# Optimization experiments

Measured on AMD Instinct MI355X. Metric: run time of the kernel, lower is better.

## Reference

```python
import jax, jax.numpy as jnp
import numpy as np
import math

D_MODEL = 256
N_HEAD = 1
C_IN = 32
B, L = 8, 2048
FACTOR = 5


def _pos_encoding(L, D):
    pos = jnp.arange(L, dtype=jnp.float32)[:, None]
    div = jnp.exp(jnp.arange(0, D, 2, dtype=jnp.float32) * (-math.log(10000.0) / D))
    pe = jnp.zeros((L, D), dtype=jnp.float32)
    pe = pe.at[:, 0::2].set(jnp.sin(pos * div))
    pe = pe.at[:, 1::2].set(jnp.cos(pos * div))
    return pe


def _layer_norm(x, g, b, eps=1e-5):
    mu = x.mean(-1, keepdims=True)
    var = ((x - mu) ** 2).mean(-1, keepdims=True)
    return (x - mu) / jnp.sqrt(var + eps) * g + b


def setup_inputs():
    key = jax.random.key(0)
    ks = jax.random.split(key, 16)
    D = D_MODEL
    s = 0.02
    p = {}
    p["x"] = jax.random.normal(ks[0], (B, L, C_IN), jnp.float32)
    sample_k = min(FACTOR * math.ceil(math.log(L)), L)  # = 40 for L=2048
    p["sample_idx"] = jax.random.randint(ks[1], (L, sample_k), 0, L)
    p["emb_w"] = jax.random.normal(ks[2], (C_IN, N_HEAD * D)) * s
    p["emb_b"] = jnp.zeros((N_HEAD * D,))
    for i, n in enumerate(["wq", "wk", "wv", "wo"]):
        p[n] = jax.random.normal(ks[3 + i], (D, D)) * s
        p["b" + n[1]] = jnp.zeros((D,))
    p["conv1_w"] = jax.random.normal(ks[7], (D, D)) * s  # Conv1d kernel=1 == linear, d_ff = d_model
    p["conv1_b"] = jnp.zeros((D,))
    p["conv2_w"] = jax.random.normal(ks[8], (D, D)) * s
    p["conv2_b"] = jnp.zeros((D,))
    for n in ["ln1", "ln2", "lnf"]:
        p[n + "_g"] = jnp.ones((D,))
        p[n + "_b"] = jnp.zeros((D,))
    p["gru_wih"] = jax.random.normal(ks[9], (3 * D, D)) * s
    p["gru_whh"] = jax.random.normal(ks[10], (3 * D, D)) * s
    p["gru_bih"] = jnp.zeros((3 * D,))
    p["gru_bhh"] = jnp.zeros((3 * D,))
    p["fc_w"] = jax.random.normal(ks[11], (D, 1)) * s
    p["fc_b"] = jnp.zeros((1,))
    return p


def _forward(x, sample_idx, emb_w, emb_b, wq, bq, wk, bk, wv, bv, wo, bo,
             conv1_w, conv1_b, conv2_w, conv2_b, ln1_g, ln1_b, ln2_g, ln2_b,
             lnf_g, lnf_b, gru_wih, gru_whh, gru_bih, gru_bhh, fc_w, fc_b):
    Bx, Lx, _ = x.shape
    H = N_HEAD
    src = x @ emb_w + emb_b + _pos_encoding(Lx, emb_w.shape[1])  # [B,L,D]
    D = src.shape[-1]
    dk = D // H

    def heads(t, w, b):
        return (t @ w + b).reshape(Bx, Lx, H, dk).transpose(0, 2, 1, 3)  # [B,H,L,dk]

    Q = heads(src, wq, bq)
    K = heads(src, wk, bk)
    V = heads(src, wv, bv)

    # ---- ProbSparse attention (Informer, non-masked) ----
    u = sample_idx.shape[1]                                  # n_top == sample_k here
    K_sample = K[:, :, sample_idx, :]                        # [B,H,L,s,dk]
    QK_s = jnp.einsum("bhld,bhlsd->bhls", Q, K_sample)
    M = QK_s.max(-1) - QK_s.sum(-1) / Lx                     # sparsity measure per query
    _, top = jax.lax.top_k(M, u)                             # [B,H,u]
    Q_red = jnp.take_along_axis(Q, top[..., None], axis=2)   # [B,H,u,dk]
    scores = jnp.einsum("bhud,bhkd->bhuk", Q_red, K) / jnp.sqrt(jnp.float32(dk))
    attn = jax.nn.softmax(scores, axis=-1)
    upd = jnp.einsum("bhuk,bhkd->bhud", attn, V)             # [B,H,u,dk]
    ctx = jnp.broadcast_to(V.mean(axis=2, keepdims=True), Q.shape)  # initial context = mean(V)
    bi = jnp.arange(Bx)[:, None, None]
    hi = jnp.arange(H)[None, :, None]
    ctx = ctx.at[bi, hi, top].set(upd)
    out = ctx.transpose(0, 2, 1, 3).reshape(Bx, Lx, D) @ wo + bo

    # ---- EncoderLayer FFN (Conv1d k=1 -> gelu -> Conv1d k=1), residuals, norms ----
    x1 = _layer_norm(src + out, ln1_g, ln1_b)
    y = jax.nn.gelu(x1 @ conv1_w + conv1_b, approximate=False)
    y = y @ conv2_w + conv2_b
    enc = _layer_norm(_layer_norm(x1 + y, ln2_g, ln2_b), lnf_g, lnf_b)

    # ---- GRU: faithful to source bug: seq-major nn.GRU fed [B,L,D] -> scans over batch dim ----
    def step(h, xt):
        gi = xt @ gru_wih.T + gru_bih
        gh = h @ gru_whh.T + gru_bhh
        ir, iz, inn = jnp.split(gi, 3, axis=-1)
        hr, hz, hn = jnp.split(gh, 3, axis=-1)
        r = jax.nn.sigmoid(ir + hr)
        z = jax.nn.sigmoid(iz + hz)
        n = jnp.tanh(inn + r * hn)
        h = (1.0 - z) * n + z * h
        return h, h

    h0 = jnp.zeros((Lx, enc.shape[-1]), enc.dtype)
    _, gru_out = jax.lax.scan(step, h0, enc)  # [B,L,D]
    return gru_out[:, -1, :] @ fc_w + fc_b    # [B,1]


def reference(x, sample_idx, emb_w, emb_b, wq, bq, wk, bk, wv, bv, wo, bo,
              conv1_w, conv1_b, conv2_w, conv2_b, ln1_g, ln1_b, ln2_g, ln2_b,
              lnf_g, lnf_b, gru_wih, gru_whh, gru_bih, gru_bhh, fc_w, fc_b):
    return _forward(x, sample_idx, emb_w, emb_b, wq, bq, wk, bk, wv, bv, wo, bo,
                    conv1_w, conv1_b, conv2_w, conv2_b, ln1_g, ln1_b, ln2_g, ln2_b,
                    lnf_g, lnf_b, gru_wih, gru_whh, gru_bih, gru_bhh, fc_w, fc_b)
```

## Files before the change

kernel.cpp:

```cpp
#include <hip/hip_runtime.h>
#include <hip/hip_bf16.h>
#include <math.h>

#define BB 8
#define LL 2048
#define CIN 32
#define DD 256
#define UU 40
#define NROW (BB*LL)
#define NSL  (NROW*DD)
#define GB 8

typedef unsigned short u16;
typedef __attribute__((ext_vector_type(8))) short short8;
typedef __attribute__((ext_vector_type(4))) float f32x4;

__device__ __forceinline__ u16 f2bf(float v) {
    unsigned u = __float_as_uint(v);
    unsigned r = (u + 0x7FFF + ((u >> 16) & 1)) >> 16;
    return (u16)r;
}
__device__ __forceinline__ float bf2f(u16 h) {
    return __uint_as_float(((unsigned)h) << 16);
}

template<int CTRL>
__device__ __forceinline__ float dpp_add(float v) {
    int s = __builtin_amdgcn_update_dpp(0, __float_as_int(v), CTRL, 0xf, 0xf, true);
    return v + __int_as_float(s);
}
__device__ __forceinline__ float row16_sum(float v) {
    v = dpp_add<0x118>(v);
    v = dpp_add<0x114>(v);
    v = dpp_add<0x112>(v);
    v = dpp_add<0x111>(v);
    return v;
}
__device__ __forceinline__ float dot4(float4 a, float4 b) {
    return a.x * b.x + a.y * b.y + a.z * b.z + a.w * b.w;
}

__global__ __launch_bounds__(256) void src_kernel(
    const float* __restrict__ x, const float* __restrict__ emb_w,
    const float* __restrict__ emb_b,
    u16* __restrict__ srch, u16* __restrict__ srcl, float* __restrict__ srcrow)
{
    __shared__ float xs[CIN];
    const int orig = blockIdx.x;
    const int b = orig & 7;
    const int l = orig >> 3;
    const int r = (b << 11) | l;
    const int d = threadIdx.x;
    if (d < CIN) xs[d] = x[(size_t)r * CIN + d];
    __syncthreads();
    float acc = emb_b[d];
#pragma unroll 8
    for (int c = 0; c < CIN; ++c) acc += xs[c] * emb_w[c * DD + d];
    const int i = d >> 1;
    const float ang = (float)l * expf((float)(2 * i) * (-9.210340371976184f / 256.0f));
    const float pe = (d & 1) ? cosf(ang) : sinf(ang);
    const float v = acc + pe;
    const u16 h = f2bf(v);
    srch[(size_t)r * DD + d] = h;
    srcl[(size_t)r * DD + d] = f2bf(v - bf2f(h));
    if (l == LL - 1) srcrow[b * DD + d] = v;
}

__global__ __launch_bounds__(256) void splitw_kernel(
    const float* __restrict__ wq, const float* __restrict__ wk,
    const float* __restrict__ wv, u16* __restrict__ whT, u16* __restrict__ wlT)
{
    const int o = blockIdx.x, n = blockIdx.y, k = threadIdx.x;
    const float* W = (o == 0) ? wq : (o == 1) ? wk : wv;
    const float v = W[(size_t)k * DD + n];
    const u16 h = f2bf(v);
    whT[((size_t)o << 16) + n * DD + k] = h;
    wlT[((size_t)o << 16) + n * DD + k] = f2bf(v - bf2f(h));
}

__global__ __launch_bounds__(256) void gemm_qkv_mfma(
    const u16* __restrict__ srch, const u16* __restrict__ srcl,
    const u16* __restrict__ whT, const u16* __restrict__ wlT,
    const float* __restrict__ bq, const float* __restrict__ bk,
    const float* __restrict__ bv,
    float* __restrict__ Qf, float* __restrict__ K, float* __restrict__ V,
    float* __restrict__ qrow)
{
    __shared__ __align__(16) u16 AhS[128][40], AlS[128][40],
                                 BhS[128][40], BlS[128][40];
    const int t = threadIdx.x;
    const int bx = blockIdx.x;
    const int mt = (bx & 7) * 16 + (bx >> 3);
    const int bm = mt * 128;
    const int bn = blockIdx.y * 128;
    const int o  = blockIdx.z;
    const u16* wh = whT + ((size_t)o << 16);
    const u16* wl = wlT + ((size_t)o << 16);
    const float* bias = (o == 0) ? bq : (o == 1) ? bk : bv;
    float* C = (o == 0) ? Qf : (o == 1) ? K : V;

    const int lane = t & 63, w = t >> 6;
    const int wr = (w >> 1) * 64, wc = (w & 1) * 64;
    const int frow = lane & 15, kg = (lane >> 4) * 8;

    f32x4 acc[4][4];
#pragma unroll
    for (int mf = 0; mf < 4; ++mf)
#pragma unroll
        for (int nf = 0; nf < 4; ++nf) acc[mf][nf] = (f32x4){0.f, 0.f, 0.f, 0.f};

    for (int ks = 0; ks < 8; ++ks) {
        const int kb = ks * 32;
#pragma unroll
        for (int e0 = 0; e0 < 512; e0 += 256) {
            const int e = e0 + t;
            const int row = e >> 2, c8 = (e & 3) * 8;
            *(short8*)&AhS[row][c8] = *(const short8*)&srch[(size_t)(bm + row) * DD + kb + c8];
            *(short8*)&AlS[row][c8] = *(const short8*)&srcl[(size_t)(bm + row) * DD + kb + c8];
            *(short8*)&BhS[row][c8] = *(const short8*)&wh[(size_t)(bn + row) * DD + kb + c8];
            *(short8*)&BlS[row][c8] = *(const short8*)&wl[(size_t)(bn + row) * DD + kb + c8];
        }
        __syncthreads();
        short8 bhr[4], blr[4];
#pragma unroll
        for (int nf = 0; nf < 4; ++nf) {
            bhr[nf] = *(const short8*)&BhS[wc + nf * 16 + frow][kg];
            blr[nf] = *(const short8*)&BlS[wc + nf * 16 + frow][kg];
        }
#pragma unroll
        for (int mf = 0; mf < 4; ++mf) {
            const short8 ah = *(const short8*)&AhS[wr + mf * 16 + frow][kg];
            const short8 al = *(const short8*)&AlS[wr + mf * 16 + frow][kg];
#pragma unroll
            for (int nf = 0; nf < 4; ++nf) {
                acc[mf][nf] = __builtin_amdgcn_mfma_f32_16x16x32_bf16(al, bhr[nf], acc[mf][nf], 0, 0, 0);
                acc[mf][nf] = __builtin_amdgcn_mfma_f32_16x16x32_bf16(ah, blr[nf], acc[mf][nf], 0, 0, 0);
                acc[mf][nf] = __builtin_amdgcn_mfma_f32_16x16x32_bf16(ah, bhr[nf], acc[mf][nf], 0, 0, 0);
            }
        }
        __syncthreads();
    }
#pragma unroll
    for (int mf = 0; mf < 4; ++mf) {
#pragma unroll
        for (int nf = 0; nf < 4; ++nf) {
#pragma unroll
            for (int r = 0; r < 4; ++r) {
                const int row = bm + wr + mf * 16 + (lane >> 4) * 4 + r;
                const int col = bn + wc + nf * 16 + (lane & 15);
                const float v = acc[mf][nf][r] + bias[col];
                C[(size_t)row * DD + col] = v;
                if (o == 0 && (row & (LL - 1)) == (LL - 1))
                    qrow[(row >> 11) * DD + col] = v;
            }
        }
    }
}

__global__ __launch_bounds__(256) void qks_probe(
    const float* __restrict__ Qf, const float* __restrict__ Kf,
    const int* __restrict__ sidx, float* __restrict__ M)
{
    __shared__ float qkp[4][4][UU];
    const int bid = blockIdx.x;
    const int b = bid & 7;
    const int grp = bid >> 3;
    const int t = threadIdx.x;
    const int wv = t >> 6;
    const int lane = t & 63;
    const int sub = lane >> 4;
    const int j = lane & 15;
    const int l = grp * 4 + wv;
    const size_t r = ((size_t)b << 11) + l;

    const int* si = sidx + (size_t)l * UU;
    const int myidx = si[lane < UU ? lane : 0];

    const float4 q = *(const float4*)&Qf[r * DD + lane * 4];
    const float* Kb = Kf + ((size_t)b << 11) * DD;

#pragma unroll
    for (int s = 0; s < UU; ++s) {
        const int idx = __builtin_amdgcn_readlane(myidx, s);
        const float4 kv = *(const float4*)&Kb[(size_t)idx * DD + lane * 4];
        float d = dot4(q, kv);
        d = row16_sum(d);
        if (j == 15) qkp[wv][sub][s] = d;
    }
    __syncthreads();
    if (t < 4) {
        float mx = -1e30f, sm = 0.0f;
#pragma unroll
        for (int s = 0; s < UU; ++s) {
            const float v = ((qkp[t][0][s] + qkp[t][1][s])
                           + qkp[t][2][s]) + qkp[t][3][s];
            mx = fmaxf(mx, v); sm += v;
        }
        M[((size_t)b << 11) + grp * 4 + t] = mx - sm * (1.0f / (float)LL);
    }
}

__global__ __launch_bounds__(256) void rank_kernel(
    const float* __restrict__ M, int* __restrict__ flag)
{
    __shared__ int redi[256];
    const int b = blockIdx.x, t = threadIdx.x;
    const float* Mb = M + (size_t)b * LL;
    const float ref = Mb[LL - 1];
    int cnt = 0;
    for (int l = t; l < LL; l += 256)
        if (l != LL - 1 && Mb[l] >= ref) cnt++;
    redi[t] = cnt; __syncthreads();
    for (int s = 128; s; s >>= 1) { if (t < s) redi[t] += redi[t + s]; __syncthreads(); }
    if (t == 0) flag[b] = (redi[0] < UU) ? 1 : 0;
}

__global__ __launch_bounds__(256) void ctx_scores(
    const float* __restrict__ qrow, const float* __restrict__ K,
    const int* __restrict__ flag, float* __restrict__ sc)
{
    const int b = blockIdx.x;
    if (!flag[b]) return;
    const int t = threadIdx.x, grp = t >> 4, j = t & 15;
    const size_t base = (size_t)b * LL * DD;
    const float4* qr = (const float4*)&qrow[b * DD];
    const float4 q0 = qr[j * 4 + 0], q1 = qr[j * 4 + 1],
                 q2 = qr[j * 4 + 2], q3 = qr[j * 4 + 3];
    const int k0 = blockIdx.y * 128 + grp * 8;
#pragma unroll
    for (int i = 0; i < 8; ++i) {
        const int k = k0 + i;
        const float4* kr = (const float4*)&K[base + (size_t)k * DD];
        float d = dot4(q0, kr[j * 4 + 0]) + dot4(q1, kr[j * 4 + 1])
                + dot4(q2, kr[j * 4 + 2]) + dot4(q3, kr[j * 4 + 3]);
        d = row16_sum(d);
        if (j == 15) sc[b * LL + k] = d * (1.0f / 16.0f);
    }
}

__global__ __launch_bounds__(256) void ctx_softmax(
    const int* __restrict__ flag, float* __restrict__ sc, float* __restrict__ ssum)
{
    __shared__ float red[256];
    const int b = blockIdx.x;
    if (!flag[b]) return;
    const int t = threadIdx.x;
    float* s = sc + b * LL;
    float lm = -1e30f;
    for (int k = t; k < LL; k += 256) lm = fmaxf(lm, s[k]);
    red[t] = lm; __syncthreads();
    for (int st = 128; st; st >>= 1) { if (t < st) red[t] = fmaxf(red[t], red[t + st]); __syncthreads(); }
    const float mx = red[0]; __syncthreads();
    float ls = 0.0f;
    for (int k = t; k < LL; k += 256) { float e = expf(s[k] - mx); s[k] = e; ls += e; }
    red[t] = ls; __syncthreads();
    for (int st = 128; st; st >>= 1) { if (t < st) red[t] += red[t + st]; __syncthreads(); }
    if (t == 0) ssum[b] = red[0];
}

__global__ __launch_bounds__(256) void ctx_pv(
    const float* __restrict__ V, const float* __restrict__ sc,
    const int* __restrict__ flag, float* __restrict__ part)
{
    const int b = blockIdx.x, slice = blockIdx.y;
    const int d = threadIdx.x;
    const size_t base = (size_t)b * LL * DD;
    const int k0 = slice * 256;
    float acc = 0.0f;
    if (flag[b]) {
#pragma unroll 4
        for (int k = k0; k < k0 + 256; ++k)
            acc += sc[b * LL + k] * V[base + (size_t)k * DD + d];
    } else {
#pragma unroll 4
        for (int k = k0; k < k0 + 256; ++k)
            acc += V[base + (size_t)k * DD + d];
    }
    part[(b * 8 + slice) * DD + d] = acc;
}

__device__ __forceinline__ float block_sum256(float v, float* red) {
    const int t = threadIdx.x;
    __syncthreads();
    red[t] = v; __syncthreads();
    for (int s = 128; s; s >>= 1) { if (t < s) red[t] += red[t + s]; __syncthreads(); }
    return red[0];
}

__global__ __launch_bounds__(256) void tail_kernel(
    const float* __restrict__ srcrow, const float* __restrict__ part,
    const float* __restrict__ ssum, const int* __restrict__ flag,
    const float* __restrict__ wo, const float* __restrict__ bo,
    const float* __restrict__ c1w, const float* __restrict__ c1b,
    const float* __restrict__ c2w, const float* __restrict__ c2b,
    const float* __restrict__ g1, const float* __restrict__ b1,
    const float* __restrict__ g2, const float* __restrict__ b2,
    const float* __restrict__ gf, const float* __restrict__ bf,
    float* __restrict__ enc)
{
    __shared__ float xs[DD];
    __shared__ float red[DD];
    const int b = blockIdx.x, d = threadIdx.x;

    float cv = 0.0f;
#pragma unroll
    for (int i = 0; i < 8; ++i) cv += part[(b * 8 + i) * DD + d];
    cv = flag[b] ? cv / ssum[b] : cv * (1.0f / (float)LL);

    xs[d] = cv; __syncthreads();
    float o = bo[d];
    for (int j = 0; j < DD; ++j) o += xs[j] * wo[j * DD + d];
    const float v = srcrow[b * DD + d] + o;

    float mu = block_sum256(v, red) * (1.0f / DD);
    float dv = v - mu;
    float var = block_sum256(dv * dv, red) * (1.0f / DD);
    const float x1 = dv * rsqrtf(var + 1e-5f) * g1[d] + b1[d];

    __syncthreads(); xs[d] = x1; __syncthreads();
    float a = c1b[d];
    for (int j = 0; j < DD; ++j) a += xs[j] * c1w[j * DD + d];
    a = 0.5f * a * (1.0f + erff(a * 0.70710678118654752f));

    __syncthreads(); xs[d] = a; __syncthreads();
    float y = c2b[d];
    for (int j = 0; j < DD; ++j) y += xs[j] * c2w[j * DD + d];

    float t2 = x1 + y;
    mu = block_sum256(t2, red) * (1.0f / DD);
    dv = t2 - mu;
    var = block_sum256(dv * dv, red) * (1.0f / DD);
    float t3 = dv * rsqrtf(var + 1e-5f) * g2[d] + b2[d];

    mu = block_sum256(t3, red) * (1.0f / DD);
    dv = t3 - mu;
    var = block_sum256(dv * dv, red) * (1.0f / DD);
    enc[b * DD + d] = dv * rsqrtf(var + 1e-5f) * gf[d] + bf[d];
}

__global__ __launch_bounds__(768) void gru_coop_kernel(
    const float* __restrict__ enc, const float* __restrict__ wih,
    const float* __restrict__ whh, const float* __restrict__ bih,
    const float* __restrict__ bhh, const float* __restrict__ fcw,
    const float* __restrict__ fcb,
    unsigned long long* __restrict__ hpub,
    float* __restrict__ out)
{
    __shared__ float whhS[96][257];
    __shared__ float encS[BB][260];
    __shared__ float giS[96][8];
    __shared__ float hS[DD];
    __shared__ float ghS[96];
    __shared__ float red[256];
    const int bid = blockIdx.x;
    if (bid & 7) return;
    const int g = bid >> 3, t = threadIdx.x;

#pragma unroll
    for (int i = 0; i < 8; ++i) {
        const int f4 = t + 768 * i;
        const int lr = f4 >> 6, c4 = f4 & 63;
        const int R = (lr >> 5) * 256 + g * 32 + (lr & 31);
        const float4 w = *(const float4*)&whh[(size_t)R * DD + c4 * 4];
        whhS[lr][c4 * 4 + 0] = w.x; whhS[lr][c4 * 4 + 1] = w.y;
        whhS[lr][c4 * 4 + 2] = w.z; whhS[lr][c4 * 4 + 3] = w.w;
    }
    for (int e = t; e < BB * DD; e += 768) encS[e >> 8][e & 255] = enc[e];
    if (t < DD) hS[t] = 0.0f;
    __syncthreads();

    {
        const int lr = t >> 3, b = t & 7;
        const int R = (lr >> 5) * 256 + g * 32 + (lr & 31);
        float acc = bih[R];
        const float4* w4 = (const float4*)&wih[(size_t)R * DD];
#pragma unroll 8
        for (int jc = 0; jc < 64; ++jc) {
            const float4 w = w4[jc];
            acc += encS[b][jc * 4 + 0] * w.x + encS[b][jc * 4 + 1] * w.y
                 + encS[b][jc * 4 + 2] * w.z + encS[b][jc * 4 + 3] * w.w;
        }
        giS[lr][b] = acc;
    }
    __syncthreads();

    for (int step = 1; step <= BB; ++step) {
        const int b = step - 1;
        const int lr = t >> 3, s = t & 7;
        float p = 0.0f;
#pragma unroll
        for (int k = 0; k < 32; ++k) {
            const int c = s * 32 + ((k + s * 4) & 31);
            p += whhS[lr][c] * hS[c];
        }
        p = dpp_add<0x114>(p); p = dpp_add<0x112>(p); p = dpp_add<0x111>(p);
        if (s == 7) ghS[lr] = p + bhh[(lr >> 5) * 256 + g * 32 + (lr & 31)];
        __syncthreads();

        if (t < 32) {
            const float r  = 1.0f / (1.0f + expf(-(giS[t][b]      + ghS[t])));
            const float z  = 1.0f / (1.0f + expf(-(giS[32 + t][b] + ghS[32 + t])));
            const float n  = tanhf(giS[64 + t][b] + r * ghS[64 + t]);
            const float hnew = (1.0f - z) * n + z * hS[g * 32 + t];
            const unsigned long long w =
                ((unsigned long long)(unsigned)step << 32) | (unsigned long long)__float_as_uint(hnew);
            __hip_atomic_store(&hpub[g * 32 + t], w, __ATOMIC_RELAXED, __HIP_MEMORY_SCOPE_AGENT);
        }
        __syncthreads();
        if (t < DD) {
            unsigned long long w;
            do {
                w = __hip_atomic_load(&hpub[t], __ATOMIC_RELAXED, __HIP_MEMORY_SCOPE_AGENT);
            } while ((int)(w >> 32) != step);
            hS[t] = __uint_as_float((unsigned)w);
        }
        __syncthreads();

        if (g == 0) {
            if (t < DD) red[t] = hS[t] * fcw[t];
            __syncthreads();
            for (int st2 = 128; st2; st2 >>= 1) { if (t < st2) red[t] += red[t + st2]; __syncthreads(); }
            if (t == 0) out[b] = red[0] + fcb[0];
            __syncthreads();
        }
    }
}

extern "C" void kernel_launch(void* const* d_in, const int* in_sizes, int n_in,
                              void* d_out, int out_size, void* d_ws, size_t ws_size,
                              hipStream_t stream)
{
    const float* x      = (const float*)d_in[0];
    const int*   sidx   = (const int*)  d_in[1];
    const float* emb_w  = (const float*)d_in[2];
    const float* emb_b  = (const float*)d_in[3];
    const float* wq     = (const float*)d_in[4];
    const float* bq     = (const float*)d_in[5];
    const float* wk     = (const float*)d_in[6];
    const float* bk     = (const float*)d_in[7];
    const float* wv     = (const float*)d_in[8];
    const float* bv     = (const float*)d_in[9];
    const float* wo     = (const float*)d_in[10];
    const float* bo     = (const float*)d_in[11];
    const float* c1w    = (const float*)d_in[12];
    const float* c1b    = (const float*)d_in[13];
    const float* c2w    = (const float*)d_in[14];
    const float* c2b    = (const float*)d_in[15];
    const float* ln1g   = (const float*)d_in[16];
    const float* ln1b   = (const float*)d_in[17];
    const float* ln2g   = (const float*)d_in[18];
    const float* ln2b   = (const float*)d_in[19];
    const float* lnfg   = (const float*)d_in[20];
    const float* lnfb   = (const float*)d_in[21];
    const float* wih    = (const float*)d_in[22];
    const float* whh    = (const float*)d_in[23];
    const float* bih    = (const float*)d_in[24];
    const float* bhh    = (const float*)d_in[25];
    const float* fcw    = (const float*)d_in[26];
    const float* fcb    = (const float*)d_in[27];

    float* ws  = (float*)d_ws;
    float* K    = ws;
    float* V    = K + NSL;
    float* Mv   = V + NSL;
    int*   flag = (int*)(Mv + NROW);
    float* sc   = (float*)(flag + 16);
    float* ssum = sc + BB * LL;
    float* part = ssum + 16;
    float* srcrow = part + BB * 8 * DD;
    float* qrow = srcrow + BB * DD;
    float* enc  = qrow + BB * DD;
    unsigned long long* hpub = (unsigned long long*)(enc + BB * DD);
    u16* srch = (u16*)(hpub + 256);
    u16* srcl = srch + NSL;
    u16* whT  = srcl + NSL;
    u16* wlT  = whT + 3 * 65536;
    float* Qf = (float*)(wlT + 3 * 65536);

    hipMemsetAsync(hpub, 0, 256 * sizeof(unsigned long long), stream);

    splitw_kernel<<<dim3(3, 256), 256, 0, stream>>>(wq, wk, wv, whT, wlT);
    src_kernel<<<NROW, 256, 0, stream>>>(x, emb_w, emb_b, srch, srcl, srcrow);
    gemm_qkv_mfma<<<dim3(128, 2, 3), 256, 0, stream>>>(srch, srcl, whT, wlT,
                                                       bq, bk, bv, Qf, K, V, qrow);
    qks_probe<<<NROW / 4, 256, 0, stream>>>(Qf, K, sidx, Mv);
    rank_kernel<<<BB, 256, 0, stream>>>(Mv, flag);
    ctx_scores<<<dim3(BB, 16), 256, 0, stream>>>(qrow, K, flag, sc);
    ctx_softmax<<<BB, 256, 0, stream>>>(flag, sc, ssum);
    ctx_pv<<<dim3(BB, 8), 256, 0, stream>>>(V, sc, flag, part);
    tail_kernel<<<BB, 256, 0, stream>>>(srcrow, part, ssum, flag, wo, bo,
                                        c1w, c1b, c2w, c2b,
                                        ln1g, ln1b, ln2g, ln2b, lnfg, lnfb, enc);
    gru_coop_kernel<<<GB * 8, 768, 0, stream>>>(enc, wih, whh, bih, bhh, fcw, fcb,
                                                hpub, (float*)d_out);
}
```

Baseline: 171.3 us.

## Double-buffer sampled K rows into LDS via async global_load_lds in probe kernel

The QK sampling probe now runs one wave per query row, with 64-thread blocks instead of four waves per block. It stages sampled K rows into shared memory in groups of four using direct global-to-LDS loads, double-buffered so the next group's gathers overlap the current group's dot products. The aim is to hide gather latency that the old version exposed on each of its 40 serial loads. In exchange it launches four times as many tiny blocks, adds explicit waitcnt and scheduling barriers, and relies on LDS-DMA semantics.

Result: slower. 184.6 us (+7.8%).

```diff
diff --git a/kernel.cpp b/kernel.cpp
--- a/kernel.cpp
+++ b/kernel.cpp
@@ -38,6 +38,15 @@
 }
 __device__ __forceinline__ float dot4(float4 a, float4 b) {
     return a.x * b.x + a.y * b.y + a.z * b.z + a.w * b.w;
+}
+__device__ __forceinline__ void gload_lds16(const float* g, float* l) {
+    __builtin_amdgcn_global_load_lds(
+        (const __attribute__((address_space(1))) float*)g,
+        (__attribute__((address_space(3))) float*)l, 16, 0, 0);
+}
+template<int N> __device__ __forceinline__ void wait_vmcnt() {
+    asm volatile("s_waitcnt vmcnt(%0)" :: "n"(N) : "memory");
+    __builtin_amdgcn_sched_barrier(0);
 }
 
 __global__ __launch_bounds__(256) void src_kernel(
@@ -157,46 +166,60 @@
     }
 }
 
-__global__ __launch_bounds__(256) void qks_probe(
+__global__ __launch_bounds__(64) void qks_probe(
     const float* __restrict__ Qf, const float* __restrict__ Kf,
     const int* __restrict__ sidx, float* __restrict__ M)
 {
-    __shared__ float qkp[4][4][UU];
+    __shared__ __align__(16) float Ks[2][4][256];
+    __shared__ float qkp[4][UU];
     const int bid = blockIdx.x;
     const int b = bid & 7;
-    const int grp = bid >> 3;
-    const int t = threadIdx.x;
-    const int wv = t >> 6;
-    const int lane = t & 63;
-    const int sub = lane >> 4;
-    const int j = lane & 15;
-    const int l = grp * 4 + wv;
+    const int l = bid >> 3;
+    const int lane = threadIdx.x;
+    const int sub = lane >> 4, j = lane & 15;
     const size_t r = ((size_t)b << 11) + l;
 
     const int* si = sidx + (size_t)l * UU;
     const int myidx = si[lane < UU ? lane : 0];
-
     const float4 q = *(const float4*)&Qf[r * DD + lane * 4];
     const float* Kb = Kf + ((size_t)b << 11) * DD;
 
 #pragma unroll
-    for (int s = 0; s < UU; ++s) {
+    for (int s = 0; s < 4; ++s) {
         const int idx = __builtin_amdgcn_readlane(myidx, s);
-        const float4 kv = *(const float4*)&Kb[(size_t)idx * DD + lane * 4];
-        float d = dot4(q, kv);
-        d = row16_sum(d);
-        if (j == 15) qkp[wv][sub][s] = d;
+        gload_lds16(Kb + (size_t)idx * DD + lane * 4, &Ks[0][s][0]);
+    }
+#pragma unroll
+    for (int g = 0; g < 10; ++g) {
+        if (g < 9) {
+#pragma unroll
+            for (int s = 0; s < 4; ++s) {
+                const int idx = __builtin_amdgcn_readlane(myidx, (g + 1) * 4 + s);
+                gload_lds16(Kb + (size_t)idx * DD + lane * 4, &Ks[(g + 1) & 1][s][0]);
+            }
+            wait_vmcnt<4>();
+        } else {
+            wait_vmcnt<0>();
+        }
+#pragma unroll
+        for (int s = 0; s < 4; ++s) {
+            const float4 kv = *(const float4*)&Ks[g & 1][s][lane * 4];
+            float d = dot4(q, kv);
+            d = row16_sum(d);
+            if (j == 15) qkp[sub][g * 4 + s] = d;
+        }
+        asm volatile("s_waitcnt lgkmcnt(0)" ::: "memory");
+        __builtin_amdgcn_sched_barrier(0);
     }
     __syncthreads();
-    if (t < 4) {
+    if (lane == 0) {
         float mx = -1e30f, sm = 0.0f;
 #pragma unroll
         for (int s = 0; s < UU; ++s) {
-            const float v = ((qkp[t][0][s] + qkp[t][1][s])
-                           + qkp[t][2][s]) + qkp[t][3][s];
+            const float v = ((qkp[0][s] + qkp[1][s]) + qkp[2][s]) + qkp[3][s];
             mx = fmaxf(mx, v); sm += v;
         }
-        M[((size_t)b << 11) + grp * 4 + t] = mx - sm * (1.0f / (float)LL);
+        M[r] = mx - sm * (1.0f / (float)LL);
     }
 }
 
@@ -483,7 +506,7 @@
     src_kernel<<<NROW, 256, 0, stream>>>(x, emb_w, emb_b, srch, srcl, srcrow);
     gemm_qkv_mfma<<<dim3(128, 2, 3), 256, 0, stream>>>(srch, srcl, whT, wlT,
                                                        bq, bk, bv, Qf, K, V, qrow);
-    qks_probe<<<NROW / 4, 256, 0, stream>>>(Qf, K, sidx, Mv);
+    qks_probe<<<NROW, 64, 0, stream>>>(Qf, K, sidx, Mv);
     rank_kernel<<<BB, 256, 0, stream>>>(Mv, flag);
     ctx_scores<<<dim3(BB, 16), 256, 0, stream>>>(qrow, K, flag, sc);
     ctx_softmax<<<BB, 256, 0, stream>>>(flag, sc, ssum);
```
